# Performance work log

Hardware: AMD Instinct MI355X
Metric: run time of the kernel (lower is better)

## Reference

```python
import jax, jax.numpy as jnp
import numpy as np

EMB = 768
HEADS = 12
HEAD_DIM = EMB // HEADS


def setup_inputs() -> dict:
    key = jax.random.key(0)
    ks = jax.random.split(key, 9)
    B, L, D = 4, 2048, EMB
    s = 1.0 / np.sqrt(D)
    return {
        "x": jax.random.normal(ks[0], (B, L, D), dtype=jnp.float32),
        "Wq": jax.random.normal(ks[1], (D, D), dtype=jnp.float32) * s,
        "bq": jnp.zeros((D,), dtype=jnp.float32),
        "Wk": jax.random.normal(ks[2], (D, D), dtype=jnp.float32) * s,
        "bk": jnp.zeros((D,), dtype=jnp.float32),
        "Wv": jax.random.normal(ks[3], (D, D), dtype=jnp.float32) * s,
        "bv": jnp.zeros((D,), dtype=jnp.float32),
        "Wo": jax.random.normal(ks[4], (D, D), dtype=jnp.float32) * s,
        "bo": jnp.zeros((D,), dtype=jnp.float32),
    }


def reference(x, Wq, bq, Wk, bk, Wv, bv, Wo, bo):
    B, L, D = x.shape
    H, hd = HEADS, HEAD_DIM
    # QKV projections -> [B, H, L, hd]
    def proj(W, b):
        return (x @ W + b).reshape(B, L, H, hd).transpose(0, 2, 1, 3)
    Q = proj(Wq, bq)
    K = proj(Wk, bk)
    V = proj(Wv, bv)
    # scores [B, H, L, L]
    scores = jnp.einsum("bhqd,bhkd->bhqk", Q, K) / jnp.sqrt(jnp.float32(hd))
    attn = jax.nn.softmax(scores, axis=-1)
    out = jnp.einsum("bhqk,bhkd->bhqd", attn, V)  # [B,H,L,hd]
    out = out.transpose(0, 2, 1, 3).reshape(B, L, D)
    return out @ Wo + bo
```

## Files before the change

### kernel.cpp

```cpp
#include <hip/hip_runtime.h>
#include <math.h>

#define TL 2048
#define TD 768
#define NH 12
#define HD 64
#define NB 4
#define MTOT (NB * TL)

typedef __bf16 bf16;
typedef __attribute__((ext_vector_type(4))) __bf16 bf16x4;
typedef __attribute__((ext_vector_type(8))) __bf16 bf16x8;
typedef __attribute__((ext_vector_type(4))) float floatx4;

#define QSCALE 0.18033688011112042f

#define MFMA16(A, B, C) __builtin_amdgcn_mfma_f32_16x16x32_bf16(A, B, C, 0, 0, 0)

__device__ __forceinline__ void gl_lds16(const void* g, void* l) {
    __builtin_amdgcn_global_load_lds(
        (const __attribute__((address_space(1))) void*)g,
        (__attribute__((address_space(3))) void*)l, 16, 0, 0);
}

__device__ __forceinline__ floatx4 exp2x4(floatx4 a) {
    floatx4 r;
    r.x = __builtin_amdgcn_exp2f(a.x);
    r.y = __builtin_amdgcn_exp2f(a.y);
    r.z = __builtin_amdgcn_exp2f(a.z);
    r.w = __builtin_amdgcn_exp2f(a.w);
    return r;
}

__device__ __forceinline__ int kperm_inv(int r) {
    return (r & 35) | (((r >> 2) & 3) << 3) | (((r >> 4) & 1) << 2);
}

__global__ __launch_bounds__(256)
void cast_x_kernel(const float* __restrict__ x, bf16* __restrict__ xb)
{
    size_t i = ((size_t)blockIdx.x * 256 + threadIdx.x) * 4;
    float4 v = *(const float4*)(x + i);
    bf16x4 o;
    o[0] = (bf16)v.x; o[1] = (bf16)v.y; o[2] = (bf16)v.z; o[3] = (bf16)v.w;
    *(bf16x4*)(xb + i) = o;
}

__global__ __launch_bounds__(256)
void transw_kernel(const float* __restrict__ W0, const float* __restrict__ W1,
                   const float* __restrict__ W2, const float* __restrict__ W3,
                   bf16* __restrict__ T0, bf16* __restrict__ T1,
                   bf16* __restrict__ T2, bf16* __restrict__ T3)
{
    const int z = blockIdx.z;
    const float* W = z == 0 ? W0 : z == 1 ? W1 : z == 2 ? W2 : W3;
    bf16*       T = z == 0 ? T0 : z == 1 ? T1 : z == 2 ? T2 : T3;
    __shared__ float Ts[64][65];
    const int t = threadIdx.x;
    const int k0 = blockIdx.x * 64, n0 = blockIdx.y * 64;
    const int rr = t >> 4, cc = (t & 15) * 4;
#pragma unroll
    for (int i = 0; i < 4; ++i) {
        int row = rr + i * 16;
        float4 v = *(const float4*)(W + (size_t)(k0 + row) * TD + n0 + cc);
        Ts[row][cc] = v.x; Ts[row][cc + 1] = v.y;
        Ts[row][cc + 2] = v.z; Ts[row][cc + 3] = v.w;
    }
    __syncthreads();
#pragma unroll
    for (int i = 0; i < 4; ++i) {
        int n = rr + i * 16;
        bf16x4 pk;
#pragma unroll
        for (int j = 0; j < 4; ++j) pk[j] = (bf16)Ts[cc + j][n];
        *(bf16x4*)(T + (size_t)(n0 + n) * TD + k0 + cc) = pk;
    }
}

__global__ __launch_bounds__(256)
void qkv_gemm(const bf16* __restrict__ xb,
              const bf16* __restrict__ Wqt, const bf16* __restrict__ Wkt,
              const bf16* __restrict__ Wvt,
              const float* __restrict__ bq, const float* __restrict__ bk,
              const float* __restrict__ bv,
              bf16* __restrict__ Q, bf16* __restrict__ K, bf16* __restrict__ Vt)
{
    __shared__ __align__(16) bf16 As[128 * 64];
    __shared__ __align__(16) bf16 Bs[128 * 64];
    __shared__ __align__(16) bf16 Eb[4][16 * 72];

    const int t = threadIdx.x;
    const int lane = t & 63, w = t >> 6;
    const int quad = lane >> 4, l16 = lane & 15;
    const int m0 = blockIdx.x * 128;
    const int n0 = blockIdx.y * 128;
    const int which = blockIdx.z;
    const bf16*  W    = which == 0 ? Wqt : which == 1 ? Wkt : Wvt;
    const float* bias = which == 0 ? bq  : which == 1 ? bk  : bv;
    const float scale = which == 0 ? QSCALE : 1.0f;

    const int rm = (w >> 1) * 64, cn = (w & 1) * 64;

    floatx4 acc[4][4];
#pragma unroll
    for (int i = 0; i < 4; ++i)
#pragma unroll
        for (int j = 0; j < 4; ++j) acc[i][j] = (floatx4){0.f, 0.f, 0.f, 0.f};

    const bf16* gA[4];
    const bf16* gB[4];
#pragma unroll
    for (int i = 0; i < 4; ++i) {
        int n = t + i * 256, r = n >> 3, s = ((n & 7) ^ (r & 7)) * 8;
        gA[i] = xb + (size_t)(m0 + r) * TD + s;
        gB[i] = W + (size_t)(n0 + r) * TD + s;
    }

    for (int kk = 0; kk < TD; kk += 64) {
#pragma unroll
        for (int i = 0; i < 4; ++i) {
            gl_lds16(gA[i] + kk, As + t * 8 + i * 2048);
            gl_lds16(gB[i] + kk, Bs + t * 8 + i * 2048);
        }
        __syncthreads();
#pragma unroll
        for (int ks = 0; ks < 2; ++ks) {
            bf16x8 af[4], bfr[4];
#pragma unroll
            for (int mb = 0; mb < 4; ++mb) {
                int r = rm + mb * 16 + l16;
                af[mb] = *(const bf16x8*)&As[r * 64 + (((ks * 4 + quad) ^ (r & 7)) * 8)];
            }
#pragma unroll
            for (int nb = 0; nb < 4; ++nb) {
                int r = cn + nb * 16 + l16;
                bfr[nb] = *(const bf16x8*)&Bs[r * 64 + (((ks * 4 + quad) ^ (r & 7)) * 8)];
            }
#pragma unroll
            for (int mb = 0; mb < 4; ++mb)
#pragma unroll
                for (int nb = 0; nb < 4; ++nb)
                    acc[mb][nb] = MFMA16(af[mb], bfr[nb], acc[mb][nb]);
        }
        __syncthreads();
    }

    float bsc[4];
#pragma unroll
    for (int nb = 0; nb < 4; ++nb)
        bsc[nb] = bias[n0 + cn + nb * 16 + l16] * scale;

    const int token0 = m0 + rm;
    const int b  = token0 >> 11;
    const int l0 = token0 & (TL - 1);
    const int h  = (n0 + cn) >> 6;
    const int bh = b * NH + h;
    bf16* Ew = Eb[w];

    if (which < 2) {
        bf16* gp = (which == 0 ? Q : K) + ((size_t)bh * TL + l0) * HD;
#pragma unroll
        for (int mb = 0; mb < 4; ++mb) {
#pragma unroll
            for (int nb = 0; nb < 4; ++nb)
#pragma unroll
                for (int r = 0; r < 4; ++r)
                    Ew[(quad * 4 + r) * 72 + nb * 16 + l16] =
                        (bf16)(acc[mb][nb][r] * scale + bsc[nb]);
#pragma unroll
            for (int i = 0; i < 2; ++i) {
                int row = i * 8 + (lane >> 3), seg = lane & 7;
                bf16x8 v = *(const bf16x8*)&Ew[row * 72 + seg * 8];
                *(bf16x8*)(gp + (size_t)(mb * 16 + row) * HD + seg * 8) = v;
            }
        }
    } else {
#pragma unroll
        for (int nb = 0; nb < 4; ++nb) {
#pragma unroll
            for (int mb = 0; mb < 4; ++mb) {
                bf16x4 pk;
#pragma unroll
                for (int r = 0; r < 4; ++r) pk[r] = (bf16)(acc[mb][nb][r] + bsc[nb]);
                *(bf16x4*)&Ew[l16 * 72 + mb * 16 + quad * 4] = pk;
            }
#pragma unroll
            for (int i = 0; i < 2; ++i) {
                int row = i * 8 + (lane >> 3), seg = lane & 7;
                bf16x8 v = *(const bf16x8*)&Ew[row * 72 + seg * 8];
                *(bf16x8*)(Vt + ((size_t)bh * HD + nb * 16 + row) * TL + l0 + seg * 8) = v;
            }
        }
    }
}

__global__ __launch_bounds__(256)
void attn_kernel(const bf16* __restrict__ Q, const bf16* __restrict__ K,
                 const bf16* __restrict__ Vt, bf16* __restrict__ O)
{
    __shared__ __align__(16) bf16 Ks[64 * 64];
    __shared__ __align__(16) bf16 Vs[64 * 64];

    const int t = threadIdx.x;
    const int lane = t & 63, w = t >> 6;
    const int quad = lane >> 4, l16 = lane & 15;

    const int n = blockIdx.y * gridDim.x + blockIdx.x;
    const int xcd = n & 7, s = n >> 3;
    const int bh = xcd * 6 + (s >> 4);
    const int q0 = (s & 15) * 128;

    const bf16* Qb = Q + (size_t)bh * TL * HD;
    const bf16* Kb = K + (size_t)bh * TL * HD;
    const bf16* Vb = Vt + (size_t)bh * HD * TL;

    const int qw = q0 + w * 32;
    bf16x8 qf[2][2];
#pragma unroll
    for (int mb = 0; mb < 2; ++mb)
#pragma unroll
        for (int ks = 0; ks < 2; ++ks)
            qf[mb][ks] = *(const bf16x8*)(Qb + (size_t)(qw + mb * 16 + l16) * HD
                                          + ks * 32 + quad * 8);

    float lrow[2] = {0.f, 0.f};
    floatx4 o[2][4];
#pragma unroll
    for (int mb = 0; mb < 2; ++mb)
#pragma unroll
        for (int db = 0; db < 4; ++db) o[mb][db] = (floatx4){0.f, 0.f, 0.f, 0.f};

    const bf16* gK[2];
    const bf16* gV[2];
#pragma unroll
    for (int i = 0; i < 2; ++i) {
        int nn = t + i * 256, r = nn >> 3, sg = ((nn & 7) ^ (r & 7)) * 8;
        gK[i] = Kb + (size_t)kperm_inv(r) * HD + sg;
        gV[i] = Vb + (size_t)r * TL + sg;
    }

    for (int kt = 0; kt < TL / 64; ++kt) {
        const int k0 = kt * 64;
        __syncthreads();
#pragma unroll
        for (int i = 0; i < 2; ++i) {
            gl_lds16(gK[i] + (size_t)k0 * HD, Ks + t * 8 + i * 2048);
            gl_lds16(gV[i] + k0,              Vs + t * 8 + i * 2048);
        }
        __syncthreads();

        floatx4 s2[2][4];
#pragma unroll
        for (int nb = 0; nb < 4; ++nb) {
            int r = nb * 16 + l16;
            bf16x8 kf0 = *(const bf16x8*)&Ks[r * 64 + ((quad ^ (r & 7)) * 8)];
            bf16x8 kf1 = *(const bf16x8*)&Ks[r * 64 + (((4 + quad) ^ (r & 7)) * 8)];
#pragma unroll
            for (int mb = 0; mb < 2; ++mb) {
                floatx4 a = (floatx4){0.f, 0.f, 0.f, 0.f};
                a = MFMA16(kf0, qf[mb][0], a);
                a = MFMA16(kf1, qf[mb][1], a);
                s2[mb][nb] = a;
            }
        }

        bf16x8 pA[2][2];
#pragma unroll
        for (int mb = 0; mb < 2; ++mb) {
#pragma unroll
            for (int ks = 0; ks < 2; ++ks) {
                floatx4 p0 = exp2x4(s2[mb][2 * ks]);
                floatx4 p1 = exp2x4(s2[mb][2 * ks + 1]);
                lrow[mb] += (p0.x + p0.y + p0.z + p0.w) + (p1.x + p1.y + p1.z + p1.w);
                bf16x8 pk;
                pk[0] = (bf16)p0.x; pk[1] = (bf16)p0.y; pk[2] = (bf16)p0.z; pk[3] = (bf16)p0.w;
                pk[4] = (bf16)p1.x; pk[5] = (bf16)p1.y; pk[6] = (bf16)p1.z; pk[7] = (bf16)p1.w;
                pA[mb][ks] = pk;
            }
        }

#pragma unroll
        for (int ks = 0; ks < 2; ++ks) {
#pragma unroll
            for (int db = 0; db < 4; ++db) {
                int r = db * 16 + l16;
                bf16x8 vf = *(const bf16x8*)&Vs[r * 64 + (((ks * 4 + quad) ^ (r & 7)) * 8)];
#pragma unroll
                for (int mb = 0; mb < 2; ++mb)
                    o[mb][db] = MFMA16(pA[mb][ks], vf, o[mb][db]);
            }
        }
    }

    const int b = bh / NH, h = bh % NH;
#pragma unroll
    for (int mb = 0; mb < 2; ++mb) {
        lrow[mb] += __shfl_xor(lrow[mb], 16);
        lrow[mb] += __shfl_xor(lrow[mb], 32);
        floatx4 inv;
#pragma unroll
        for (int r = 0; r < 4; ++r)
            inv[r] = 1.0f / __shfl(lrow[mb], (lane & 48) | (quad * 4 + r));
#pragma unroll
        for (int db = 0; db < 4; ++db)
#pragma unroll
            for (int r = 0; r < 4; ++r) {
                int l = qw + mb * 16 + quad * 4 + r;
                O[((size_t)b * TL + l) * TD + h * HD + db * 16 + l16] =
                    (bf16)(o[mb][db][r] * inv[r]);
            }
    }
}

__global__ __launch_bounds__(256)
void oproj_gemm(const bf16* __restrict__ A, const bf16* __restrict__ Wt,
                const float* __restrict__ bo, float* __restrict__ out)
{
    __shared__ __align__(16) bf16 As[128 * 64];
    __shared__ __align__(16) bf16 Bs[128 * 64];
    __shared__ __align__(16) float Ef[4][16 * 68];

    const int t = threadIdx.x;
    const int lane = t & 63, w = t >> 6;
    const int quad = lane >> 4, l16 = lane & 15;
    const int m0 = blockIdx.x * 128;
    const int n0 = blockIdx.y * 128;
    const int rm = (w >> 1) * 64, cn = (w & 1) * 64;

    floatx4 acc[4][4];
#pragma unroll
    for (int i = 0; i < 4; ++i)
#pragma unroll
        for (int j = 0; j < 4; ++j) acc[i][j] = (floatx4){0.f, 0.f, 0.f, 0.f};

    const bf16* gA[4];
    const bf16* gB[4];
#pragma unroll
    for (int i = 0; i < 4; ++i) {
        int n = t + i * 256, r = n >> 3, s = ((n & 7) ^ (r & 7)) * 8;
        gA[i] = A + (size_t)(m0 + r) * TD + s;
        gB[i] = Wt + (size_t)(n0 + r) * TD + s;
    }

    for (int kk = 0; kk < TD; kk += 64) {
#pragma unroll
        for (int i = 0; i < 4; ++i) {
            gl_lds16(gA[i] + kk, As + t * 8 + i * 2048);
            gl_lds16(gB[i] + kk, Bs + t * 8 + i * 2048);
        }
        __syncthreads();
#pragma unroll
        for (int ks = 0; ks < 2; ++ks) {
            bf16x8 af[4], bfr[4];
#pragma unroll
            for (int mb = 0; mb < 4; ++mb) {
                int r = rm + mb * 16 + l16;
                af[mb] = *(const bf16x8*)&As[r * 64 + (((ks * 4 + quad) ^ (r & 7)) * 8)];
            }
#pragma unroll
            for (int nb = 0; nb < 4; ++nb) {
                int r = cn + nb * 16 + l16;
                bfr[nb] = *(const bf16x8*)&Bs[r * 64 + (((ks * 4 + quad) ^ (r & 7)) * 8)];
            }
#pragma unroll
            for (int mb = 0; mb < 4; ++mb)
#pragma unroll
                for (int nb = 0; nb < 4; ++nb)
                    acc[mb][nb] = MFMA16(af[mb], bfr[nb], acc[mb][nb]);
        }
        __syncthreads();
    }

    float bb[4];
#pragma unroll
    for (int nb = 0; nb < 4; ++nb) bb[nb] = bo[n0 + cn + nb * 16 + l16];

    float* Ew = Ef[w];
#pragma unroll
    for (int mb = 0; mb < 4; ++mb) {
#pragma unroll
        for (int nb = 0; nb < 4; ++nb)
#pragma unroll
            for (int r = 0; r < 4; ++r)
                Ew[(quad * 4 + r) * 68 + nb * 16 + l16] = acc[mb][nb][r] + bb[nb];
#pragma unroll
        for (int i = 0; i < 4; ++i) {
            int row = i * 4 + (lane >> 4), seg = lane & 15;
            float4 v = *(const float4*)&Ew[row * 68 + seg * 4];
            *(float4*)(out + (size_t)(m0 + rm + mb * 16 + row) * TD + n0 + cn + seg * 4) = v;
        }
    }
}

extern "C" void kernel_launch(void* const* d_in, const int* in_sizes, int n_in,
                              void* d_out, int out_size, void* d_ws, size_t ws_size,
                              hipStream_t stream)
{
    const float* x  = (const float*)d_in[0];
    const float* Wq = (const float*)d_in[1];
    const float* bq = (const float*)d_in[2];
    const float* Wk = (const float*)d_in[3];
    const float* bk = (const float*)d_in[4];
    const float* Wv = (const float*)d_in[5];
    const float* bv = (const float*)d_in[6];
    const float* Wo = (const float*)d_in[7];
    const float* bo = (const float*)d_in[8];

    const size_t NXE = (size_t)MTOT * TD;
    const size_t NWE = (size_t)TD * TD;

    bf16* xb  = (bf16*)d_ws;
    bf16* Wqt = xb + NXE;
    bf16* Wkt = Wqt + NWE;
    bf16* Wvt = Wkt + NWE;
    bf16* Wot = Wvt + NWE;
    bf16* Qb  = Wot + NWE;
    bf16* Kb  = Qb + NXE;
    bf16* Vtb = Kb + NXE;
    bf16* Ob  = Vtb + NXE;

    cast_x_kernel<<<6144, 256, 0, stream>>>(x, xb);
    transw_kernel<<<dim3(12, 12, 4), 256, 0, stream>>>(Wq, Wk, Wv, Wo,
                                                       Wqt, Wkt, Wvt, Wot);
    qkv_gemm<<<dim3(MTOT / 128, TD / 128, 3), 256, 0, stream>>>(
        xb, Wqt, Wkt, Wvt, bq, bk, bv, Qb, Kb, Vtb);
    attn_kernel<<<dim3(TL / 128, NB * NH), 256, 0, stream>>>(Qb, Kb, Vtb, Ob);
    oproj_gemm<<<dim3(MTOT / 128, TD / 128), 256, 0, stream>>>(Ob, Wot, bo,
                                                               (float*)d_out);
}
```

Baseline: 215.8 us.

## Double-buffer K/V tiles in LDS and prefetch next tile during compute

The attention kernel now keeps two LDS buffers each for K and V. It issues the async global-to-LDS loads for tile kt+1 before computing on tile kt, so load latency overlaps the MFMA and exp work and one barrier per iteration goes away. It also raises wave priority with s_setprio around the two MFMA phases. In exchange, LDS use doubles, which may limit how many blocks can stay resident per CU.

```diff
diff --git a/kernel.cpp b/kernel.cpp
--- a/kernel.cpp
+++ b/kernel.cpp
@@ -198,8 +198,8 @@
 void attn_kernel(const bf16* __restrict__ Q, const bf16* __restrict__ K,
                  const bf16* __restrict__ Vt, bf16* __restrict__ O)
 {
-    __shared__ __align__(16) bf16 Ks[64 * 64];
-    __shared__ __align__(16) bf16 Vs[64 * 64];
+    __shared__ __align__(16) bf16 Ks[2][64 * 64];
+    __shared__ __align__(16) bf16 Vs[2][64 * 64];
 
     const int t = threadIdx.x;
     const int lane = t & 63, w = t >> 6;
@@ -223,13 +223,6 @@
             qf[mb][ks] = *(const bf16x8*)(Qb + (size_t)(qw + mb * 16 + l16) * HD
                                           + ks * 32 + quad * 8);
 
-    float lrow[2] = {0.f, 0.f};
-    floatx4 o[2][4];
-#pragma unroll
-    for (int mb = 0; mb < 2; ++mb)
-#pragma unroll
-        for (int db = 0; db < 4; ++db) o[mb][db] = (floatx4){0.f, 0.f, 0.f, 0.f};
-
     const bf16* gK[2];
     const bf16* gV[2];
 #pragma unroll
@@ -239,22 +232,44 @@
         gV[i] = Vb + (size_t)r * TL + sg;
     }
 
+#pragma unroll
+    for (int i = 0; i < 2; ++i) {
+        gl_lds16(gK[i], Ks[0] + t * 8 + i * 2048);
+        gl_lds16(gV[i], Vs[0] + t * 8 + i * 2048);
+    }
+
+    float lrow[2] = {0.f, 0.f};
+    floatx4 o[2][4];
+#pragma unroll
+    for (int mb = 0; mb < 2; ++mb)
+#pragma unroll
+        for (int db = 0; db < 4; ++db) o[mb][db] = (floatx4){0.f, 0.f, 0.f, 0.f};
+
+    __syncthreads();
+
     for (int kt = 0; kt < TL / 64; ++kt) {
-        const int k0 = kt * 64;
-        __syncthreads();
-#pragma unroll
-        for (int i = 0; i < 2; ++i) {
-            gl_lds16(gK[i] + (size_t)k0 * HD, Ks + t * 8 + i * 2048);
-            gl_lds16(gV[i] + k0,              Vs + t * 8 + i * 2048);
-        }
-        __syncthreads();
+        const int cur = kt & 1;
+        const bf16* Kc = Ks[cur];
+        const bf16* Vc = Vs[cur];
+
+        if (kt + 1 < TL / 64) {
+            const int k0n = (kt + 1) * 64;
+            bf16* Kn = Ks[cur ^ 1];
+            bf16* Vn = Vs[cur ^ 1];
+#pragma unroll
+            for (int i = 0; i < 2; ++i) {
+                gl_lds16(gK[i] + (size_t)k0n * HD, Kn + t * 8 + i * 2048);
+                gl_lds16(gV[i] + k0n,              Vn + t * 8 + i * 2048);
+            }
+        }
 
         floatx4 s2[2][4];
+        __builtin_amdgcn_s_setprio(1);
 #pragma unroll
         for (int nb = 0; nb < 4; ++nb) {
             int r = nb * 16 + l16;
-            bf16x8 kf0 = *(const bf16x8*)&Ks[r * 64 + ((quad ^ (r & 7)) * 8)];
-            bf16x8 kf1 = *(const bf16x8*)&Ks[r * 64 + (((4 + quad) ^ (r & 7)) * 8)];
+            bf16x8 kf0 = *(const bf16x8*)&Kc[r * 64 + ((quad ^ (r & 7)) * 8)];
+            bf16x8 kf1 = *(const bf16x8*)&Kc[r * 64 + (((4 + quad) ^ (r & 7)) * 8)];
 #pragma unroll
             for (int mb = 0; mb < 2; ++mb) {
                 floatx4 a = (floatx4){0.f, 0.f, 0.f, 0.f};
@@ -263,6 +278,7 @@
                 s2[mb][nb] = a;
             }
         }
+        __builtin_amdgcn_s_setprio(0);
 
         bf16x8 pA[2][2];
 #pragma unroll
@@ -279,17 +295,21 @@
             }
         }
 
+        __builtin_amdgcn_s_setprio(1);
 #pragma unroll
         for (int ks = 0; ks < 2; ++ks) {
 #pragma unroll
             for (int db = 0; db < 4; ++db) {
                 int r = db * 16 + l16;
-                bf16x8 vf = *(const bf16x8*)&Vs[r * 64 + (((ks * 4 + quad) ^ (r & 7)) * 8)];
+                bf16x8 vf = *(const bf16x8*)&Vc[r * 64 + (((ks * 4 + quad) ^ (r & 7)) * 8)];
 #pragma unroll
                 for (int mb = 0; mb < 2; ++mb)
                     o[mb][db] = MFMA16(pA[mb][ks], vf, o[mb][db]);
             }
         }
+        __builtin_amdgcn_s_setprio(0);
+
+        __syncthreads();
     }
 
     const int b = bh / NH, h = bh % NH;
```

New measurement: 237.2 us. 9.9% more time.
